# Kernel tuning notes

Measured on AMD Instinct MI355X. Metric: run time of the kernel, lower is better.

Reference implementation:

```python
import jax, jax.numpy as jnp
import numpy as np
import math

B, L, DIM, H = 1, 2048, 512, 8
D = DIM // H
STEPS = 1024
TWO_PI = 2.0 * math.pi
CHUNK = 64  # matches torch chunk_size


def setup_inputs() -> dict:
    key = jax.random.key(0)
    ks = jax.random.split(key, 6)
    x = jax.random.normal(ks[0], (B, L, DIM), jnp.float32)
    W_qs = jax.random.normal(ks[1], (DIM, 2 * DIM), jnp.float32) * 0.02
    b_qs = jnp.zeros((2 * DIM,), jnp.float32)
    ln_w = jnp.ones((2 * DIM,), jnp.float32)
    ln_b = jnp.zeros((2 * DIM,), jnp.float32)
    freq = jax.random.normal(ks[2], (H,), jnp.float32) * 0.02
    phase_shift = jax.random.normal(ks[3], (H,), jnp.float32) * 0.02
    W_out = jax.random.normal(ks[4], (DIM, DIM), jnp.float32) * 0.02
    b_out = jnp.zeros((DIM,), jnp.float32)
    # buffer: cos(linspace(0, 2pi, 1024)) exactly as in _init_lookup_tables
    cos_table = jnp.cos(jnp.linspace(0.0, TWO_PI, STEPS)).astype(jnp.float32)
    return dict(x=x, W_qs=W_qs, b_qs=b_qs, ln_w=ln_w, ln_b=ln_b,
                freq=freq, phase_shift=phase_shift, W_out=W_out, b_out=b_out,
                cos_table=cos_table)


def _forward(x, W_qs, b_qs, ln_w, ln_b, freq, phase_shift, W_out, b_out, cos_table):
    # quantum state preparation (shared module applied to same x => q == k states)
    qs = x @ W_qs + b_qs                                  # [B,L,2*DIM]
    mu = jnp.mean(qs, axis=-1, keepdims=True)
    var = jnp.var(qs, axis=-1, keepdims=True)
    qs = (qs - mu) / jnp.sqrt(var + 1e-5) * ln_w + ln_b    # LayerNorm(2*dim)
    amp, phase = jnp.split(qs, 2, axis=-1)                 # [B,L,DIM] each
    amp = jax.nn.sigmoid(amp)
    amp = amp / (jnp.sqrt(jnp.sum(amp ** 2, axis=-1, keepdims=True)) + 1e-8)
    phase = jnp.tanh(phase) * math.pi

    to_heads = lambda t: t.reshape(B, L, H, D).transpose(0, 2, 1, 3)  # [B,H,L,D]
    q_amp = to_heads(amp)
    q_phase = to_heads(phase)
    v = to_heads(x)

    NC = L // CHUNK
    qa_c = q_amp.reshape(B, H, NC, CHUNK, D).transpose(2, 0, 1, 3, 4)   # [NC,B,H,C,D]
    qp_c = q_phase.reshape(B, H, NC, CHUNK, D).transpose(2, 0, 1, 3, 4)
    f = freq[None, :, None, None, None]
    s = phase_shift[None, :, None, None, None]

    def chunk(carry, qc):
        qa, qp = qc                                         # [B,H,C,D]
        # pairwise per-dim phase interference via lookup table
        pd = (qp[:, :, :, None, :] - q_phase[:, :, None, :, :]) * f + s  # [B,H,C,L,D]
        idx = ((pd / TWO_PI * STEPS) % STEPS).astype(jnp.int32)
        interf = cos_table[idx]
        score = jnp.sum(qa[:, :, :, None, :] * q_amp[:, :, None, :, :] * interf,
                        axis=-1)                            # [B,H,C,L]
        return carry, score

    _, scores = jax.lax.scan(jax.checkpoint(chunk), 0, (qa_c, qp_c))
    scores = scores.transpose(1, 2, 0, 3, 4).reshape(B, H, L, L)
    attn = jax.nn.softmax(scores / math.sqrt(D), axis=-1)
    out = jnp.einsum('bhqk,bhkd->bhqd', attn, v)            # [B,H,L,D]
    out = out.transpose(0, 2, 1, 3).reshape(B, L, DIM)
    return out @ W_out + b_out


def reference(x, W_qs, b_qs, ln_w, ln_b, freq, phase_shift, W_out, b_out, cos_table):
    return _forward(x, W_qs, b_qs, ln_w, ln_b, freq, phase_shift, W_out, b_out, cos_table)
```

## Files before the change

### kernel.cpp

```cpp
#include <hip/hip_runtime.h>
#include <cstdint>
#include <cstddef>


typedef __attribute__((ext_vector_type(8))) short short8;
typedef __attribute__((ext_vector_type(4))) float f32x4;

#define MFMA16(a, b, c) __builtin_amdgcn_mfma_f32_16x16x32_bf16((a), (b), (c), 0, 0, 0)

static constexpr size_t B_ATTB = 0;
static constexpr size_t B_UB   = (size_t)2 * 1024 * 1024;
static constexpr size_t B_WB   = B_UB + (size_t)4 * 1024 * 1024;
static constexpr size_t B_VT   = B_WB + (size_t)4 * 1024 * 1024;
static constexpr size_t B_WQT  = B_VT + (size_t)2 * 1024 * 1024;
static constexpr size_t B_WOT  = B_WQT + (size_t)1 * 1024 * 1024;

__device__ __forceinline__ unsigned short f2bf(float f) {
  unsigned u = __float_as_uint(f);
  return (unsigned short)((u + 0x7FFFu + ((u >> 16) & 1u)) >> 16);
}

__global__ __launch_bounds__(256) void k_prep(const float* __restrict__ x,
    const float* __restrict__ Wq, const float* __restrict__ Wo,
    unsigned short* __restrict__ vT, unsigned short* __restrict__ WqTp,
    unsigned short* __restrict__ WoT) {
  __shared__ float tl[64 * 65];
  const int t = threadIdx.x, b = blockIdx.x;
  if (b < 256) {
    const int i0 = (b >> 3) * 64, h = b & 7;
    #pragma unroll
    for (int it = 0; it < 16; ++it) {
      int n = t + 256 * it;
      int r = n >> 6, c = n & 63;
      tl[r * 65 + c] = x[(size_t)(i0 + r) * 512 + h * 64 + c];
    }
    __syncthreads();
    #pragma unroll
    for (int it = 0; it < 16; ++it) {
      int n = t + 256 * it;
      int d = n >> 6, ii = n & 63;
      vT[(size_t)(h * 64 + d) * 2048 + i0 + ii] = f2bf(tl[ii * 65 + d]);
    }
  } else if (b < 384) {
    const int bb = b - 256;
    const int k0 = (bb >> 4) * 64, n0 = (bb & 15) * 64;
    #pragma unroll
    for (int it = 0; it < 16; ++it) {
      int n = t + 256 * it;
      int r = n >> 6, c = n & 63;
      tl[r * 65 + c] = Wq[(size_t)(k0 + r) * 1024 + n0 + c];
    }
    __syncthreads();
    #pragma unroll
    for (int it = 0; it < 16; ++it) {
      int n = t + 256 * it;
      int rr = n >> 6, cc = n & 63;
      int nn = n0 + rr, kk = k0 + cc;
      int nt = nn >> 4, mm = nn & 15;
      int kc32 = kk >> 5, qd = (kk >> 3) & 3, j = kk & 7;
      WqTp[(((size_t)nt * 16 + kc32) * 64 + qd * 16 + mm) * 8 + j] =
          f2bf(tl[cc * 65 + rr]);
    }
  } else {
    const int bb = b - 384;
    const int k0 = (bb >> 3) * 64, n0 = (bb & 7) * 64;
    #pragma unroll
    for (int it = 0; it < 16; ++it) {
      int n = t + 256 * it;
      int r = n >> 6, c = n & 63;
      tl[r * 65 + c] = Wo[(size_t)(k0 + r) * 512 + n0 + c];
    }
    __syncthreads();
    #pragma unroll
    for (int it = 0; it < 16; ++it) {
      int n = t + 256 * it;
      int rr = n >> 6, cc = n & 63;
      WoT[(size_t)(n0 + rr) * 512 + k0 + cc] = f2bf(tl[cc * 65 + rr]);
    }
  }
}

__global__ __launch_bounds__(512) void k_qs_ln(const float* __restrict__ x,
    const unsigned short* __restrict__ WqTp, const float* __restrict__ bq,
    const float* __restrict__ lnw, const float* __restrict__ lnb,
    const float* __restrict__ fr, const float* __restrict__ psh,
    unsigned short* __restrict__ Ub, unsigned short* __restrict__ Wb) {
  __shared__ __align__(16) unsigned short s_a[16 * 520];
  __shared__ float s_amp[16 * 516];
  __shared__ float red[8 * 16 * 2];
  __shared__ float red2[4 * 16];
  const int r0 = blockIdx.x * 16, t = threadIdx.x;
  const int w = t >> 6, lane = t & 63, m = lane & 15, quad = lane >> 4;
  {
    const int row = t >> 5, cs = (t & 31) * 16;
    const float4* xr = (const float4*)(x + (size_t)(r0 + row) * 512 + cs);
    unsigned short tmp[16];
    #pragma unroll
    for (int q4 = 0; q4 < 4; ++q4) {
      float4 v = xr[q4];
      tmp[q4 * 4 + 0] = f2bf(v.x); tmp[q4 * 4 + 1] = f2bf(v.y);
      tmp[q4 * 4 + 2] = f2bf(v.z); tmp[q4 * 4 + 3] = f2bf(v.w);
    }
    *(short8*)(s_a + row * 520 + cs)     = *(short8*)(tmp);
    *(short8*)(s_a + row * 520 + cs + 8) = *(short8*)(tmp + 8);
  }
  __syncthreads();
  f32x4 acc[8] = {{0,0,0,0},{0,0,0,0},{0,0,0,0},{0,0,0,0},
                  {0,0,0,0},{0,0,0,0},{0,0,0,0},{0,0,0,0}};
  for (int kc32 = 0; kc32 < 16; ++kc32) {
    short8 af = *(const short8*)(s_a + m * 520 + kc32 * 32 + quad * 8);
    const unsigned short* bp =
        WqTp + (((size_t)(w * 8) * 16 + kc32) * 64 + lane) * 8;
    #pragma unroll
    for (int nt = 0; nt < 8; ++nt) {
      short8 bf = *(const short8*)(bp + (size_t)nt * 8192);
      acc[nt] = MFMA16(af, bf, acc[nt]);
    }
  }
  #pragma unroll
  for (int nt = 0; nt < 8; ++nt) {
    float bv = bq[w * 128 + nt * 16 + m];
    #pragma unroll
    for (int r = 0; r < 4; ++r) acc[nt][r] += bv;
  }
  float s1[4] = {0, 0, 0, 0}, s2[4] = {0, 0, 0, 0};
  #pragma unroll
  for (int r = 0; r < 4; ++r)
    #pragma unroll
    for (int nt = 0; nt < 8; ++nt) {
      float v = acc[nt][r];
      s1[r] += v; s2[r] += v * v;
    }
  #pragma unroll
  for (int off = 1; off < 16; off <<= 1)
    #pragma unroll
    for (int r = 0; r < 4; ++r) {
      s1[r] += __shfl_xor(s1[r], off, 64);
      s2[r] += __shfl_xor(s2[r], off, 64);
    }
  if (m == 0)
    #pragma unroll
    for (int r = 0; r < 4; ++r) {
      red[(w * 16 + quad * 4 + r) * 2]     = s1[r];
      red[(w * 16 + quad * 4 + r) * 2 + 1] = s2[r];
    }
  __syncthreads();
  float mu[4], rstd[4];
  #pragma unroll
  for (int r = 0; r < 4; ++r) {
    int row = quad * 4 + r;
    float S = 0, S2 = 0;
    #pragma unroll
    for (int wp = 0; wp < 8; ++wp) {
      S  += red[(wp * 16 + row) * 2];
      S2 += red[(wp * 16 + row) * 2 + 1];
    }
    mu[r] = S * (1.0f / 1024.0f);
    float var = S2 * (1.0f / 1024.0f) - mu[r] * mu[r];
    rstd[r] = 1.0f / sqrtf(var + 1e-5f);
  }
  float y[8][4];
  #pragma unroll
  for (int nt = 0; nt < 8; ++nt) {
    int c = w * 128 + nt * 16 + m;
    float gw = lnw[c], gb = lnb[c];
    #pragma unroll
    for (int r = 0; r < 4; ++r)
      y[nt][r] = (acc[nt][r] - mu[r]) * rstd[r] * gw + gb;
  }
  const float PI_F = 3.14159265358979323846f;
  if (w < 4) {
    float a[8][4];
    float na[4] = {0, 0, 0, 0};
    #pragma unroll
    for (int nt = 0; nt < 8; ++nt)
      #pragma unroll
      for (int r = 0; r < 4; ++r) {
        float v = __builtin_amdgcn_rcpf(1.0f + __expf(-y[nt][r]));
        a[nt][r] = v;
        na[r] += v * v;
      }
    #pragma unroll
    for (int off = 1; off < 16; off <<= 1)
      #pragma unroll
      for (int r = 0; r < 4; ++r) na[r] += __shfl_xor(na[r], off, 64);
    if (m == 0)
      #pragma unroll
      for (int r = 0; r < 4; ++r) red2[w * 16 + quad * 4 + r] = na[r];
    __syncthreads();
    float inv[4];
    #pragma unroll
    for (int r = 0; r < 4; ++r) {
      int row = quad * 4 + r;
      float N = red2[row] + red2[16 + row] + red2[32 + row] + red2[48 + row];
      inv[r] = 1.0f / (sqrtf(N) + 1e-8f);
    }
    #pragma unroll
    for (int nt = 0; nt < 8; ++nt)
      #pragma unroll
      for (int r = 0; r < 4; ++r)
        s_amp[(quad * 4 + r) * 516 + w * 128 + nt * 16 + m] = a[nt][r] * inv[r];
    __syncthreads();
  } else {
    float p[8][4];
    #pragma unroll
    for (int nt = 0; nt < 8; ++nt)
      #pragma unroll
      for (int r = 0; r < 4; ++r) {
        float e2 = __expf(2.0f * y[nt][r]);
        p[nt][r] = (1.0f - 2.0f * __builtin_amdgcn_rcpf(e2 + 1.0f)) * PI_F;
      }
    __syncthreads();
    __syncthreads();
    const double GAM = 1024.0 / 1023.0;
    const int hbase = (w - 4) * 2;
    float c1[2], s1g[2];
    #pragma unroll
    for (int hh = 0; hh < 2; ++hh) {
      c1[hh]  = (float)((double)fr[hbase + hh] * GAM);
      s1g[hh] = (float)((double)psh[hbase + hh] * GAM);
    }
    #pragma unroll
    for (int nt = 0; nt < 8; ++nt) {
      const int hh = nt >> 2;
      const int pc = (w - 4) * 128 + nt * 16 + m;
      const int d = pc & 63;
      #pragma unroll
      for (int r = 0; r < 4; ++r) {
        const int i = r0 + quad * 4 + r;
        float af = s_amp[(quad * 4 + r) * 516 + pc];
        float A = fmaf(p[nt][r], c1[hh], s1g[hh]);
        float Bp = p[nt][r] * c1[hh];
        float cA, sA, cB, sB;
        __sincosf(A, &sA, &cA);
        __sincosf(Bp, &sB, &cB);
        size_t base = ((size_t)(hbase + hh) * 2048 + i) * 128 + d;
        Ub[base]      = f2bf(af * cA);
        Ub[base + 64] = f2bf(af * sA);
        Wb[base]      = f2bf(af * cB);
        Wb[base + 64] = f2bf(af * sB);
      }
    }
  }
}

__global__ __launch_bounds__(512, 2) void k_flash5(const unsigned short* __restrict__ Ub,
    const unsigned short* __restrict__ Wb, const unsigned short* __restrict__ vT,
    unsigned short* __restrict__ attb) {
  __shared__ __align__(16) unsigned char s_w[2][128 * 272];
  __shared__ __align__(16) unsigned char s_v[2][64 * 272];
  __shared__ __align__(16) unsigned char s_p[8][16 * 144];
  const int qt = blockIdx.x, h = blockIdx.y;
  const int q0 = qt * 64;
  const int t = threadIdx.x;
  const int wave = t >> 6, lane = t & 63;
  const int qw = wave & 3, kw = wave >> 2;
  const int m = lane & 15, quad = lane >> 4;
  const int sr = t >> 2, sp = t & 3;
  const int vr = t >> 3, vp = t & 7;
  unsigned char* s_pw = s_p[wave];
  short8 afr[4];
  const unsigned short* urow = Ub + ((size_t)h * 2048 + q0 + qw * 16 + m) * 128;
  #pragma unroll
  for (int fs = 0; fs < 4; ++fs)
    afr[fs] = *(const short8*)(urow + fs * 32 + quad * 8);
  short8 ones;
  #pragma unroll
  for (int j = 0; j < 8; ++j) ones[j] = (short)0x3F80;
  f32x4 oacc[4] = {{0,0,0,0},{0,0,0,0},{0,0,0,0},{0,0,0,0}};
  f32x4 dacc = {0, 0, 0, 0};
  const unsigned short* wgbase = Wb + (size_t)h * 2048 * 128 + (size_t)sr * 128;
  const unsigned short* vgbase = vT + ((size_t)h * 64 + vr) * 2048;
  #pragma unroll
  for (int it = 0; it < 4; ++it)
    *(short8*)(s_w[0] + sr * 272 + sp * 64 + it * 16) =
      *(const short8*)(wgbase + sp * 32 + it * 8);
  #pragma unroll
  for (int it = 0; it < 2; ++it)
    *(short8*)(s_v[0] + vr * 272 + vp * 32 + it * 16) =
      *(const short8*)(vgbase + vp * 16 + it * 8);
  __syncthreads();
  for (int kt = 0; kt < 16; ++kt) {
    const int cur = kt & 1;
    short8 wst[4], vst[2];
    const bool has = (kt < 15);
    if (has) {
      const unsigned short* wg = wgbase + (size_t)(kt + 1) * 128 * 128;
      #pragma unroll
      for (int it = 0; it < 4; ++it)
        wst[it] = *(const short8*)(wg + sp * 32 + it * 8);
      const unsigned short* vg = vgbase + (kt + 1) * 128;
      #pragma unroll
      for (int it = 0; it < 2; ++it)
        vst[it] = *(const short8*)(vg + vp * 16 + it * 8);
    }
    f32x4 sc[4] = {{0,0,0,0},{0,0,0,0},{0,0,0,0},{0,0,0,0}};
    #pragma unroll
    for (int ksub = 0; ksub < 4; ++ksub) {
      const int krow = kw * 64 + ksub * 16 + m;
      #pragma unroll
      for (int fs = 0; fs < 4; ++fs) {
        short8 bfr = *(const short8*)(s_w[cur] + krow * 272 + fs * 64 + quad * 16);
        sc[ksub] = MFMA16(afr[fs], bfr, sc[ksub]);
      }
    }
    #pragma unroll
    for (int ksub = 0; ksub < 4; ++ksub)
      #pragma unroll
      for (int r = 0; r < 4; ++r) {
        float p = __expf(sc[ksub][r] * 0.125f);
        *(unsigned short*)(s_pw + (quad * 4 + r) * 144 + (ksub * 16 + m) * 2) = f2bf(p);
      }
    #pragma unroll
    for (int k2 = 0; k2 < 2; ++k2) {
      short8 pf = *(const short8*)(s_pw + m * 144 + k2 * 64 + quad * 16);
      dacc = MFMA16(pf, ones, dacc);
      #pragma unroll
      for (int dt = 0; dt < 4; ++dt) {
        short8 vf = *(const short8*)(s_v[cur] + (dt * 16 + m) * 272 +
                                     kw * 128 + k2 * 64 + quad * 16);
        oacc[dt] = MFMA16(pf, vf, oacc[dt]);
      }
    }
    if (has) {
      #pragma unroll
      for (int it = 0; it < 4; ++it)
        *(short8*)(s_w[cur ^ 1] + sr * 272 + sp * 64 + it * 16) = wst[it];
      #pragma unroll
      for (int it = 0; it < 2; ++it)
        *(short8*)(s_v[cur ^ 1] + vr * 272 + vp * 32 + it * 16) = vst[it];
    }
    __syncthreads();
  }
  float* s_ored = (float*)(s_w[0]);
  float* s_dred = (float*)(s_w[0] + 16384);
  if (kw == 1) {
    #pragma unroll
    for (int dt = 0; dt < 4; ++dt)
      #pragma unroll
      for (int r = 0; r < 4; ++r)
        s_ored[qw * 1024 + (quad * 4 + r) * 64 + dt * 16 + m] = oacc[dt][r];
    if (m == 0) {
      #pragma unroll
      for (int r = 0; r < 4; ++r)
        s_dred[qw * 16 + quad * 4 + r] = dacc[r];
    }
  }
  __syncthreads();
  if (kw == 0) {
    float invd[4];
    #pragma unroll
    for (int r = 0; r < 4; ++r)
      invd[r] = 1.0f / (dacc[r] + s_dred[qw * 16 + quad * 4 + r]);
    #pragma unroll
    for (int dt = 0; dt < 4; ++dt)
      #pragma unroll
      for (int r = 0; r < 4; ++r) {
        float o = oacc[dt][r] + s_ored[qw * 1024 + (quad * 4 + r) * 64 + dt * 16 + m];
        attb[(size_t)(q0 + qw * 16 + quad * 4 + r) * 512 + h * 64 + dt * 16 + m] =
            f2bf(o * invd[r]);
      }
  }
}

__global__ __launch_bounds__(256) void k_gemm(const unsigned short* __restrict__ A,
    const unsigned short* __restrict__ Bt, const float* __restrict__ bias,
    float* __restrict__ C, int N) {
  __shared__ __align__(16) unsigned char sm[2 * 64 * 136];
  unsigned char* s_a = sm;
  unsigned char* s_b = sm + 64 * 136;
  const int m0 = blockIdx.x * 64, n0 = blockIdx.y * 64;
  const int t = threadIdx.x;
  const int wave = t >> 6, lane = t & 63;
  const int m = lane & 15, quad = lane >> 4;
  const int sr = t >> 2, spart = t & 3;
  f32x4 acc[4] = {{0,0,0,0},{0,0,0,0},{0,0,0,0},{0,0,0,0}};
  for (int kc = 0; kc < 512; kc += 64) {
    #pragma unroll
    for (int it = 0; it < 2; ++it) {
      *(short8*)(s_a + sr * 136 + spart * 32 + it * 16) =
        *(const short8*)(A + (size_t)(m0 + sr) * 512 + kc + spart * 16 + it * 8);
      *(short8*)(s_b + sr * 136 + spart * 32 + it * 16) =
        *(const short8*)(Bt + (size_t)(n0 + sr) * 512 + kc + spart * 16 + it * 8);
    }
    __syncthreads();
    #pragma unroll
    for (int k2 = 0; k2 < 2; ++k2) {
      short8 af = *(const short8*)(s_a + (wave * 16 + m) * 136 + k2 * 64 + quad * 16);
      #pragma unroll
      for (int nt = 0; nt < 4; ++nt) {
        short8 bf = *(const short8*)(s_b + (nt * 16 + m) * 136 + k2 * 64 + quad * 16);
        acc[nt] = MFMA16(af, bf, acc[nt]);
      }
    }
    __syncthreads();
  }
  #pragma unroll
  for (int nt = 0; nt < 4; ++nt) {
    int col = n0 + nt * 16 + m;
    float bv = bias[col];
    #pragma unroll
    for (int r = 0; r < 4; ++r) {
      int row = m0 + wave * 16 + quad * 4 + r;
      C[(size_t)row * N + col] = acc[nt][r] + bv;
    }
  }
}

extern "C" void kernel_launch(void* const* d_in, const int* in_sizes, int n_in,
                              void* d_out, int out_size, void* d_ws, size_t ws_size,
                              hipStream_t stream) {
  (void)in_sizes; (void)n_in; (void)out_size; (void)ws_size;
  const float* x   = (const float*)d_in[0];
  const float* Wq  = (const float*)d_in[1];
  const float* bq  = (const float*)d_in[2];
  const float* lnw = (const float*)d_in[3];
  const float* lnb = (const float*)d_in[4];
  const float* fr  = (const float*)d_in[5];
  const float* ps  = (const float*)d_in[6];
  const float* Wo  = (const float*)d_in[7];
  const float* bo  = (const float*)d_in[8];
  char* ws = (char*)d_ws;
  unsigned short* attb = (unsigned short*)(ws + B_ATTB);
  unsigned short* Ub   = (unsigned short*)(ws + B_UB);
  unsigned short* Wb   = (unsigned short*)(ws + B_WB);
  unsigned short* vT   = (unsigned short*)(ws + B_VT);
  unsigned short* WqTp = (unsigned short*)(ws + B_WQT);
  unsigned short* WoT  = (unsigned short*)(ws + B_WOT);
  float* out = (float*)d_out;

  k_prep<<<448, 256, 0, stream>>>(x, Wq, Wo, vT, WqTp, WoT);
  k_qs_ln<<<128, 512, 0, stream>>>(x, WqTp, bq, lnw, lnb, fr, ps, Ub, Wb);
  k_flash5<<<dim3(32, 8), 512, 0, stream>>>(Ub, Wb, vT, attb);
  k_gemm<<<dim3(32, 8), 256, 0, stream>>>(attb, WoT, bo, out, 512);
}
```

Before: 150.6 us.

## Repartition flash attention waves by key rows for scores and head-dim halves for PV

After: 147.0 us. 2.4% less time.

```diff
diff --git a/kernel.cpp b/kernel.cpp
--- a/kernel.cpp
+++ b/kernel.cpp
@@ -244,30 +244,32 @@
   }
 }
 
-__global__ __launch_bounds__(512, 2) void k_flash5(const unsigned short* __restrict__ Ub,
+__global__ __launch_bounds__(512, 1) void k_flash6(const unsigned short* __restrict__ Ub,
     const unsigned short* __restrict__ Wb, const unsigned short* __restrict__ vT,
     unsigned short* __restrict__ attb) {
   __shared__ __align__(16) unsigned char s_w[2][128 * 272];
   __shared__ __align__(16) unsigned char s_v[2][64 * 272];
-  __shared__ __align__(16) unsigned char s_p[8][16 * 144];
+  __shared__ __align__(16) unsigned char s_p[2][64 * 272];
   const int qt = blockIdx.x, h = blockIdx.y;
   const int q0 = qt * 64;
   const int t = threadIdx.x;
   const int wave = t >> 6, lane = t & 63;
-  const int qw = wave & 3, kw = wave >> 2;
+  const int qg = wave & 3, dh = wave >> 2;
   const int m = lane & 15, quad = lane >> 4;
   const int sr = t >> 2, sp = t & 3;
   const int vr = t >> 3, vp = t & 7;
-  unsigned char* s_pw = s_p[wave];
-  short8 afr[4];
-  const unsigned short* urow = Ub + ((size_t)h * 2048 + q0 + qw * 16 + m) * 128;
-  #pragma unroll
-  for (int fs = 0; fs < 4; ++fs)
-    afr[fs] = *(const short8*)(urow + fs * 32 + quad * 8);
+  short8 afr[4][4];
+  #pragma unroll
+  for (int g = 0; g < 4; ++g) {
+    const unsigned short* urow = Ub + ((size_t)h * 2048 + q0 + g * 16 + m) * 128;
+    #pragma unroll
+    for (int fs = 0; fs < 4; ++fs)
+      afr[g][fs] = *(const short8*)(urow + fs * 32 + quad * 8);
+  }
   short8 ones;
   #pragma unroll
   for (int j = 0; j < 8; ++j) ones[j] = (short)0x3F80;
-  f32x4 oacc[4] = {{0,0,0,0},{0,0,0,0},{0,0,0,0},{0,0,0,0}};
+  f32x4 oacc[2] = {{0,0,0,0},{0,0,0,0}};
   f32x4 dacc = {0, 0, 0, 0};
   const unsigned short* wgbase = Wb + (size_t)h * 2048 * 128 + (size_t)sr * 128;
   const unsigned short* vgbase = vT + ((size_t)h * 64 + vr) * 2048;
@@ -296,32 +298,27 @@
     }
     f32x4 sc[4] = {{0,0,0,0},{0,0,0,0},{0,0,0,0},{0,0,0,0}};
     #pragma unroll
-    for (int ksub = 0; ksub < 4; ++ksub) {
-      const int krow = kw * 64 + ksub * 16 + m;
-      #pragma unroll
-      for (int fs = 0; fs < 4; ++fs) {
-        short8 bfr = *(const short8*)(s_w[cur] + krow * 272 + fs * 64 + quad * 16);
-        sc[ksub] = MFMA16(afr[fs], bfr, sc[ksub]);
+    for (int fs = 0; fs < 4; ++fs) {
+      short8 bfr = *(const short8*)(s_w[cur] + (wave * 16 + m) * 272 + fs * 64 + quad * 16);
+      #pragma unroll
+      for (int g = 0; g < 4; ++g)
+        sc[g] = MFMA16(afr[g][fs], bfr, sc[g]);
+    }
+    #pragma unroll
+    for (int g = 0; g < 4; ++g)
+      #pragma unroll
+      for (int r = 0; r < 4; ++r) {
+        float p = __expf(sc[g][r] * 0.125f);
+        *(unsigned short*)(s_p[cur] + (g * 16 + quad * 4 + r) * 272 +
+                           (wave * 16 + m) * 2) = f2bf(p);
       }
-    }
-    #pragma unroll
-    for (int ksub = 0; ksub < 4; ++ksub)
-      #pragma unroll
-      for (int r = 0; r < 4; ++r) {
-        float p = __expf(sc[ksub][r] * 0.125f);
-        *(unsigned short*)(s_pw + (quad * 4 + r) * 144 + (ksub * 16 + m) * 2) = f2bf(p);
-      }
-    #pragma unroll
-    for (int k2 = 0; k2 < 2; ++k2) {
-      short8 pf = *(const short8*)(s_pw + m * 144 + k2 * 64 + quad * 16);
-      dacc = MFMA16(pf, ones, dacc);
-      #pragma unroll
-      for (int dt = 0; dt < 4; ++dt) {
-        short8 vf = *(const short8*)(s_v[cur] + (dt * 16 + m) * 272 +
-                                     kw * 128 + k2 * 64 + quad * 16);
-        oacc[dt] = MFMA16(pf, vf, oacc[dt]);
-      }
-    }
+    short8 vf[4][2];
+    #pragma unroll
+    for (int k2 = 0; k2 < 4; ++k2)
+      #pragma unroll
+      for (int dt = 0; dt < 2; ++dt)
+        vf[k2][dt] = *(const short8*)(s_v[cur] + (dh * 32 + dt * 16 + m) * 272 +
+                                      k2 * 64 + quad * 16);
     if (has) {
       #pragma unroll
       for (int it = 0; it < 4; ++it)
@@ -331,36 +328,24 @@
         *(short8*)(s_v[cur ^ 1] + vr * 272 + vp * 32 + it * 16) = vst[it];
     }
     __syncthreads();
-  }
-  float* s_ored = (float*)(s_w[0]);
-  float* s_dred = (float*)(s_w[0] + 16384);
-  if (kw == 1) {
-    #pragma unroll
-    for (int dt = 0; dt < 4; ++dt)
-      #pragma unroll
-      for (int r = 0; r < 4; ++r)
-        s_ored[qw * 1024 + (quad * 4 + r) * 64 + dt * 16 + m] = oacc[dt][r];
-    if (m == 0) {
-      #pragma unroll
-      for (int r = 0; r < 4; ++r)
-        s_dred[qw * 16 + quad * 4 + r] = dacc[r];
-    }
-  }
-  __syncthreads();
-  if (kw == 0) {
-    float invd[4];
+    #pragma unroll
+    for (int k2 = 0; k2 < 4; ++k2) {
+      short8 pf = *(const short8*)(s_p[cur] + (qg * 16 + m) * 272 + k2 * 64 + quad * 16);
+      dacc = MFMA16(pf, ones, dacc);
+      #pragma unroll
+      for (int dt = 0; dt < 2; ++dt)
+        oacc[dt] = MFMA16(pf, vf[k2][dt], oacc[dt]);
+    }
+  }
+  float invd[4];
+  #pragma unroll
+  for (int r = 0; r < 4; ++r) invd[r] = 1.0f / dacc[r];
+  #pragma unroll
+  for (int dt = 0; dt < 2; ++dt)
     #pragma unroll
     for (int r = 0; r < 4; ++r)
-      invd[r] = 1.0f / (dacc[r] + s_dred[qw * 16 + quad * 4 + r]);
-    #pragma unroll
-    for (int dt = 0; dt < 4; ++dt)
-      #pragma unroll
-      for (int r = 0; r < 4; ++r) {
-        float o = oacc[dt][r] + s_ored[qw * 1024 + (quad * 4 + r) * 64 + dt * 16 + m];
-        attb[(size_t)(q0 + qw * 16 + quad * 4 + r) * 512 + h * 64 + dt * 16 + m] =
-            f2bf(o * invd[r]);
-      }
-  }
+      attb[(size_t)(q0 + qg * 16 + quad * 4 + r) * 512 + h * 64 +
+           dh * 32 + dt * 16 + m] = f2bf(oacc[dt][r] * invd[r]);
 }
 
 __global__ __launch_bounds__(256) void k_gemm(const unsigned short* __restrict__ A,
@@ -431,6 +416,6 @@
 
   k_prep<<<448, 256, 0, stream>>>(x, Wq, Wo, vT, WqTp, WoT);
   k_qs_ln<<<128, 512, 0, stream>>>(x, WqTp, bq, lnw, lnb, fr, ps, Ub, Wb);
-  k_flash5<<<dim3(32, 8), 512, 0, stream>>>(Ub, Wb, vT, attb);
+  k_flash6<<<dim3(32, 8), 512, 0, stream>>>(Ub, Wb, vT, attb);
   k_gemm<<<dim3(32, 8), 256, 0, stream>>>(attb, WoT, bo, out, 512);
 }
```
